# Optimization experiments

Hardware: AMD Instinct MI355X
Metric: run time of the kernel (lower is better)

The kernel has to match this reference:

```python
import jax, jax.numpy as jnp
import numpy as np

D, HS, HE, E, K = 1024, 2048, 1024, 8, 2   # d_model, shared hidden (d_ff//2), expert hidden (d_ff//4), n_experts, top_k
B, T = 4, 1024
N_SHARED = 1


def setup_inputs() -> dict:
    key = jax.random.key(0)
    ks = jax.random.split(key, 9)
    g = lambda k, shape, s: jax.random.normal(k, shape, jnp.float32) * s
    return {
        "x": g(ks[0], (B, T, D), 1.0),
        "t_emb": g(ks[1], (B, D), 1.0),
        "router_W": g(ks[2], (2 * D, E), 0.01),      # torch Linear(2C->E, bias=False), std=0.01 init
        "router_bias": jnp.zeros((E,), jnp.float32),  # load-balance bias buffer
        "w1": g(ks[3], (D, HS), 0.02),                # shared expert SwiGLU
        "w3": g(ks[4], (D, HS), 0.02),
        "w2": g(ks[5], (HS, D), 0.02),
        "W1e": g(ks[6], (E, D, HE), 0.02),            # routed experts, Linear->GELU->Linear
        "W2e": g(ks[7], (E, HE, D), 0.02),
    }


def reference(x, t_emb, router_W, router_bias, w1, w3, w2, W1e, W2e):
    Bb, Tt, C = x.shape
    xf = x.reshape(-1, C)                                              # [N, C]
    tf = jnp.broadcast_to(t_emb[:, None, :], (Bb, Tt, C)).reshape(-1, C)
    N = xf.shape[0]

    shared = (jax.nn.silu(xf @ w1) * (xf @ w3)) @ w2                   # [N, C]

    # router affinity (sigmoid, fp32)
    s = jax.nn.sigmoid((jnp.concatenate([xf, tf], axis=-1) @ router_W).astype(jnp.float32))
    sel_scores = s + router_bias                                       # [N, E]
    _, topk_idx = jax.lax.top_k(sel_scores, K)                         # [N, K]

    # gates normalized over selected raw affinities
    s_sel = jnp.take_along_axis(s, topk_idx, axis=1)                   # [N, K]
    denom = s_sel.sum(axis=1, keepdims=True)
    gates = jnp.where(denom > 1e-9, s_sel / (denom + 1e-9), 1.0 / K).astype(x.dtype)

    # combine weights [N, E]: scatter gates to selected experts
    combine = jnp.zeros((N, E), x.dtype).at[jnp.arange(N)[:, None], topk_idx].add(gates)

    # dense expert evaluation (reference form of grouped GEMM + scatter-combine)
    h = jax.nn.gelu(jnp.einsum('nc,ech->enh', xf, W1e), approximate=False)  # [E, N, He]
    y = jnp.einsum('enh,ehc->enc', h, W2e)                                   # [E, N, C]
    routed = jnp.einsum('ne,enc->nc', combine, y)                            # [N, C]

    return ((shared + routed) / (N_SHARED + K)).reshape(Bb, Tt, C)
```

## Files before the change

kernel.cpp:

```cpp
#include <hip/hip_runtime.h>
#include <hip/hip_bf16.h>
#include <math.h>

#define D_MODEL 1024
#define HS 2048
#define HE 1024
#define NEXP 8
#define NTOK 4096
#define NSLOT 8192

typedef __attribute__((ext_vector_type(4))) float f32x4;
typedef __attribute__((ext_vector_type(8))) short bf16x8;

__device__ __forceinline__ short f2b(float f) {
  __hip_bfloat16 h = __float2bfloat16(f);
  return *reinterpret_cast<short*>(&h);
}
__device__ __forceinline__ float b2f(short s) {
  return __bfloat162float(*reinterpret_cast<__hip_bfloat16*>(&s));
}

__device__ __forceinline__ void gl_lds16(const short* g, short* l) {
  __builtin_amdgcn_global_load_lds(
      (const __attribute__((address_space(1))) void*)g,
      (__attribute__((address_space(3))) void*)l, 16, 0, 0);
}

__device__ __forceinline__ void tr_tile(const float* __restrict__ in,
                                        short* __restrict__ out, int R, int C,
                                        int bx, int by, int bz, int rmap,
                                        float (*tile)[69], int t) {
  const int c0 = bx * 64;
  const int r0 = by * 64;
  const size_t bo = (size_t)bz * R * C;
  const int lr = t >> 4;
  const int lc4 = (t & 15) * 4;
#pragma unroll
  for (int i = 0; i < 4; i++) {
    const float4 v = *(const float4*)&in[bo + (size_t)(r0 + lr + i * 16) * C + c0 + lc4];
    tile[lc4 + 0][lr + i * 16] = v.x;
    tile[lc4 + 1][lr + i * 16] = v.y;
    tile[lc4 + 2][lr + i * 16] = v.z;
    tile[lc4 + 3][lr + i * 16] = v.w;
  }
  __syncthreads();
#pragma unroll
  for (int i = 0; i < 4; i++) {
    const int oc = (t >> 4) + i * 16;
    const int or4 = (t & 15) * 4;
    short4 o;
    o.x = f2b(tile[oc][or4 + 0]);
    o.y = f2b(tile[oc][or4 + 1]);
    o.z = f2b(tile[oc][or4 + 2]);
    o.w = f2b(tile[oc][or4 + 3]);
    const int c = c0 + oc;
    size_t orow;
    if (rmap == 0) orow = bo + (size_t)c * R;
    else orow = (size_t)((c >> 5) * 64 + (rmap == 2 ? 32 : 0) + (c & 31)) * R;
    *(short4*)&out[orow + r0 + or4] = o;
  }
}

__global__ __launch_bounds__(256) void tr_w13(const float* __restrict__ w1,
                                              const float* __restrict__ w3,
                                              short* __restrict__ w13I) {
  __shared__ float tile[64][69];
  const int z = blockIdx.z;
  tr_tile(z ? w3 : w1, w13I, D_MODEL, HS, blockIdx.x, blockIdx.y, 0, z ? 2 : 1,
          tile, threadIdx.x);
}

__global__ __launch_bounds__(256) void tr_w2(const float* __restrict__ w2,
                                             short* __restrict__ w2T) {
  __shared__ float tile[64][69];
  tr_tile(w2, w2T, HS, D_MODEL, blockIdx.x, blockIdx.y, 0, 0, tile, threadIdx.x);
}

__global__ __launch_bounds__(256) void tr_exp(const float* __restrict__ W1e,
                                              const float* __restrict__ W2e,
                                              short* __restrict__ W1eT,
                                              short* __restrict__ W2eT) {
  __shared__ float tile[64][69];
  const int z = blockIdx.z;
  if (z < 8)
    tr_tile(W1e, W1eT, D_MODEL, HE, blockIdx.x, blockIdx.y, z, 0, tile, threadIdx.x);
  else
    tr_tile(W2e, W2eT, HE, D_MODEL, blockIdx.x, blockIdx.y, z - 8, 0, tile, threadIdx.x);
}

__global__ __launch_bounds__(256) void router_kernel(
    const float* __restrict__ x, const float* __restrict__ temb,
    const float* __restrict__ rw, const float* __restrict__ rbias,
    short* __restrict__ xb, int* __restrict__ topk, float* __restrict__ gates) {
  const int t = (blockIdx.x * 256 + threadIdx.x) >> 6;
  const int lane = threadIdx.x & 63;
  const float* xr = x + (size_t)t * D_MODEL;
  const float* tr = temb + (size_t)(t >> 10) * D_MODEL;
  float acc[NEXP] = {};
#pragma unroll
  for (int i = 0; i < 4; i++) {
    const int j = i * 256 + lane * 4;
    const float4 xv = *(const float4*)&xr[j];
    const float4 tv = *(const float4*)&tr[j];
    short4 o;
    o.x = f2b(xv.x); o.y = f2b(xv.y); o.z = f2b(xv.z); o.w = f2b(xv.w);
    *(short4*)&xb[(size_t)t * D_MODEL + j] = o;
    const float* wx = rw + (size_t)j * NEXP;
    const float* wt = rw + (size_t)(D_MODEL + j) * NEXP;
    const float xa[4] = {xv.x, xv.y, xv.z, xv.w};
    const float ta[4] = {tv.x, tv.y, tv.z, tv.w};
#pragma unroll
    for (int u = 0; u < 4; u++)
#pragma unroll
      for (int e = 0; e < NEXP; e++)
        acc[e] += xa[u] * wx[u * NEXP + e] + ta[u] * wt[u * NEXP + e];
  }
#pragma unroll
  for (int off = 32; off; off >>= 1)
#pragma unroll
    for (int e = 0; e < NEXP; e++) acc[e] += __shfl_xor(acc[e], off);
  if (lane == 0) {
    float s[NEXP], sel[NEXP];
#pragma unroll
    for (int e = 0; e < NEXP; e++) {
      s[e] = 1.f / (1.f + expf(-acc[e]));
      sel[e] = s[e] + rbias[e];
    }
    int i0 = 0;
#pragma unroll
    for (int e = 1; e < NEXP; e++) if (sel[e] > sel[i0]) i0 = e;
    int i1 = (i0 == 0) ? 1 : 0;
#pragma unroll
    for (int e = 0; e < NEXP; e++) if (e != i0 && sel[e] > sel[i1]) i1 = e;
    float s0 = s[i0], s1 = s[i1], den = s0 + s1;
    float g0, g1;
    if (den > 1e-9f) { g0 = s0 / (den + 1e-9f); g1 = s1 / (den + 1e-9f); }
    else { g0 = 0.5f; g1 = 0.5f; }
    topk[t * 2] = i0; topk[t * 2 + 1] = i1;
    gates[t * 2] = g0; gates[t * 2 + 1] = g1;
  }
}

__global__ __launch_bounds__(1024) void group_kernel(const int* __restrict__ topk,
                                                     int* __restrict__ perm,
                                                     int* __restrict__ offs,
                                                     int* __restrict__ te,
                                                     int* __restrict__ tm,
                                                     int* __restrict__ ntile) {
  __shared__ int cnt[NEXP], cur[NEXP];
  const int t = threadIdx.x;
  if (t < NEXP) cnt[t] = 0;
  __syncthreads();
  int mye[8];
#pragma unroll
  for (int i = 0; i < 8; i++) {
    mye[i] = topk[i * 1024 + t];
    atomicAdd(&cnt[mye[i]], 1);
  }
  __syncthreads();
  if (t == 0) {
    int a = 0;
    for (int e = 0; e < NEXP; e++) { offs[e] = a; cur[e] = a; a += cnt[e]; }
    offs[NEXP] = a;
    int nt = 0;
    for (int e = 0; e < NEXP; e++)
      for (int m0 = 0; m0 < cnt[e]; m0 += 128) { te[nt] = e; tm[nt] = m0; nt++; }
    ntile[0] = nt;
  }
  __syncthreads();
#pragma unroll
  for (int i = 0; i < 8; i++) {
    int pos = atomicAdd(&cur[mye[i]], 1);
    perm[pos] = i * 1024 + t;
  }
}

template <int MODE, int NT>
__global__ __launch_bounds__(256, 2) void g128(
    const short* __restrict__ A, const short* __restrict__ B, void* __restrict__ Cout,
    const int* __restrict__ perm, const int* __restrict__ offs,
    const float* __restrict__ gates, const int* __restrict__ te,
    const int* __restrict__ tm, const int* __restrict__ ntile,
    const short* __restrict__ yb) {
  extern __shared__ short lds[];
  const int td = threadIdx.x;
  const int K = NT * 64;

  int m_panel = 0, n_panel = 0, e = 0, m0 = 0, rbeg = 0, rend = 0, bxn = 0;
  const short* Bbase;
  if (MODE == 0) {
    const int xcd = blockIdx.x & 7, w = blockIdx.x >> 3;
    n_panel = xcd * 4 + (w >> 5);
    m_panel = w & 31;
    Bbase = B + (size_t)n_panel * 128 * K;
  } else if (MODE == 3) {
    const int xcd = blockIdx.x & 7, slot = blockIdx.x >> 3;
    n_panel = slot & 7;
    m_panel = xcd * 4 + (slot >> 3);
    Bbase = B + (size_t)n_panel * 128 * K;
  } else {
    const int ty = blockIdx.x >> 3;
    if (ty >= ntile[0]) return;
    bxn = blockIdx.x & 7;
    e = te[ty];
    m0 = tm[ty];
    rbeg = offs[e]; rend = offs[e + 1];
    Bbase = B + ((size_t)e * 1024 + bxn * 128) * K;
  }

  const int srow = td >> 3;
  const int colsw8 = ((td & 7) ^ (srow & 7)) * 8;
  const short* ap[4];
  const short* bp[4];
#pragma unroll
  for (int u = 0; u < 4; u++) {
    const int trow = u * 32 + srow;
    int grow;
    if (MODE == 0) grow = m_panel * 128 + trow;
    else if (MODE == 1) grow = perm[min(rbeg + m0 + trow, rend - 1)] >> 1;
    else if (MODE == 2) grow = min(rbeg + m0 + trow, rend - 1);
    else grow = m_panel * 128 + trow;
    ap[u] = A + (size_t)grow * K + colsw8;
    bp[u] = Bbase + (size_t)trow * K + colsw8;
  }

#define STAGE(t_, b_)                                                      \
  do {                                                                     \
    gl_lds16(ap[0] + (t_) * 64, lds + (b_) * 16384 + td * 8);              \
    gl_lds16(ap[1] + (t_) * 64, lds + (b_) * 16384 + 2048 + td * 8);       \
    gl_lds16(ap[2] + (t_) * 64, lds + (b_) * 16384 + 4096 + td * 8);       \
    gl_lds16(ap[3] + (t_) * 64, lds + (b_) * 16384 + 6144 + td * 8);       \
    gl_lds16(bp[0] + (t_) * 64, lds + (b_) * 16384 + 8192 + td * 8);       \
    gl_lds16(bp[1] + (t_) * 64, lds + (b_) * 16384 + 10240 + td * 8);      \
    gl_lds16(bp[2] + (t_) * 64, lds + (b_) * 16384 + 12288 + td * 8);      \
    gl_lds16(bp[3] + (t_) * 64, lds + (b_) * 16384 + 14336 + td * 8);      \
  } while (0)

  const int l = td & 63;
  const int wv = td >> 6;
  const int wm = (wv >> 1) * 64, wn = (wv & 1) * 64;
  const int lr = l & 15;
  const int swzk0 = ((0 + (l >> 4) * 16) ^ ((l & 7) << 4)) >> 1;
  const int swzk1 = ((64 + (l >> 4) * 16) ^ ((l & 7) << 4)) >> 1;

#define LDA(mf_, swz_) (*(const bf16x8*)&Ah[(unsigned)(((mf_)*16 + lr) * 64) + (swz_)])
#define LDB(nf_, swz_) (*(const bf16x8*)&Bh[(unsigned)(((nf_)*16 + lr) * 64) + (swz_)])
#define MMROW(mf_, a_)                                                                 \
  acc[mf_][0] = __builtin_amdgcn_mfma_f32_16x16x32_bf16(a_, b0, acc[mf_][0], 0, 0, 0); \
  acc[mf_][1] = __builtin_amdgcn_mfma_f32_16x16x32_bf16(a_, b1, acc[mf_][1], 0, 0, 0); \
  acc[mf_][2] = __builtin_amdgcn_mfma_f32_16x16x32_bf16(a_, b2, acc[mf_][2], 0, 0, 0); \
  acc[mf_][3] = __builtin_amdgcn_mfma_f32_16x16x32_bf16(a_, b3, acc[mf_][3], 0, 0, 0)

  f32x4 acc[4][4] = {};

  STAGE(0, 0);
  for (int t = 0; t < NT; ++t) {
    const int p = t & 1, q = p ^ 1;
    const short* Ah = lds + p * 16384 + wm * 64;
    const short* Bh = lds + p * 16384 + 8192 + wn * 64;
    if (t < NT - 1) {
      STAGE(t + 1, q);
      asm volatile("s_waitcnt vmcnt(8)" ::: "memory");
    } else {
      asm volatile("s_waitcnt vmcnt(0)" ::: "memory");
    }
    __builtin_amdgcn_s_barrier();
    {
      bf16x8 b0, b1, b2, b3, a0, a1, a2, a3;
      b0 = LDB(0, swzk0); b1 = LDB(1, swzk0); b2 = LDB(2, swzk0); b3 = LDB(3, swzk0);
      a0 = LDA(0, swzk0); a1 = LDA(1, swzk0); a2 = LDA(2, swzk0); a3 = LDA(3, swzk0);
      __builtin_amdgcn_s_setprio(1);
      MMROW(0, a0); MMROW(1, a1); MMROW(2, a2); MMROW(3, a3);
      __builtin_amdgcn_s_setprio(0);
      b0 = LDB(0, swzk1); b1 = LDB(1, swzk1); b2 = LDB(2, swzk1); b3 = LDB(3, swzk1);
      a0 = LDA(0, swzk1); a1 = LDA(1, swzk1); a2 = LDA(2, swzk1); a3 = LDA(3, swzk1);
      __builtin_amdgcn_s_setprio(1);
      MMROW(0, a0); MMROW(1, a1); MMROW(2, a2); MMROW(3, a3);
      __builtin_amdgcn_s_setprio(0);
    }
    __builtin_amdgcn_sched_barrier(0);
    __builtin_amdgcn_s_barrier();
  }

  const int rq = (l >> 4) * 4;
  if (MODE == 0) {
#pragma unroll
    for (int mf = 0; mf < 4; mf++)
#pragma unroll
      for (int j = 0; j < 4; j++) {
        const int row = m_panel * 128 + wm + mf * 16 + rq + j;
        short* Up = (short*)Cout + (size_t)row * HS + n_panel * 64 + (wn >> 1) + lr;
#pragma unroll
        for (int nf = 0; nf < 2; nf++) {
          const float a = acc[mf][nf][j];
          const float b = acc[mf][nf + 2][j];
          Up[nf * 16] = f2b(a / (1.f + expf(-a)) * b);
        }
      }
  } else if (MODE == 1) {
#pragma unroll
    for (int mf = 0; mf < 4; mf++)
#pragma unroll
      for (int j = 0; j < 4; j++) {
        const int gi = rbeg + m0 + wm + mf * 16 + rq + j;
        if (gi < rend) {
          short* Cp = (short*)Cout + (size_t)gi * HE + bxn * 128 + wn + lr;
#pragma unroll
          for (int nf = 0; nf < 4; nf++) {
            const float v = acc[mf][nf][j];
            Cp[nf * 16] = f2b(0.5f * v * (1.0f + erff(v * 0.70710678118654752f)));
          }
        }
      }
  } else if (MODE == 2) {
#pragma unroll
    for (int mf = 0; mf < 4; mf++)
#pragma unroll
      for (int j = 0; j < 4; j++) {
        const int gi = rbeg + m0 + wm + mf * 16 + rq + j;
        if (gi < rend) {
          const int slot = perm[gi];
          const float g = gates[slot];
          short* Cp = (short*)Cout + (size_t)slot * D_MODEL + bxn * 128 + wn + lr;
#pragma unroll
          for (int nf = 0; nf < 4; nf++) Cp[nf * 16] = f2b(g * acc[mf][nf][j]);
        }
      }
  } else {
    const float inv3 = 1.0f / 3.0f;
#pragma unroll
    for (int mf = 0; mf < 4; mf++)
#pragma unroll
      for (int j = 0; j < 4; j++) {
        const int tok = m_panel * 128 + wm + mf * 16 + rq + j;
        const int colb = n_panel * 128 + wn + lr;
        const short* y0p = yb + (size_t)(tok * 2) * D_MODEL + colb;
        const short* y1p = yb + (size_t)(tok * 2 + 1) * D_MODEL + colb;
        float* Op = (float*)Cout + (size_t)tok * D_MODEL + colb;
#pragma unroll
        for (int nf = 0; nf < 4; nf++) {
          Op[nf * 16] = (acc[mf][nf][j] + b2f(y0p[nf * 16]) + b2f(y1p[nf * 16])) * inv3;
        }
      }
  }
#undef STAGE
#undef LDA
#undef LDB
#undef MMROW
}

extern "C" void kernel_launch(void* const* d_in, const int* in_sizes, int n_in,
                              void* d_out, int out_size, void* d_ws, size_t ws_size,
                              hipStream_t stream) {
  const float* x = (const float*)d_in[0];
  const float* temb = (const float*)d_in[1];
  const float* rw = (const float*)d_in[2];
  const float* rbias = (const float*)d_in[3];
  const float* w1 = (const float*)d_in[4];
  const float* w3 = (const float*)d_in[5];
  const float* w2 = (const float*)d_in[6];
  const float* W1e = (const float*)d_in[7];
  const float* W2e = (const float*)d_in[8];
  float* out = (float*)d_out;

  const size_t MB = 1ull << 20;
  char* w = (char*)d_ws;
  short* xb    = (short*)(w + 0 * MB);
  short* w13I  = (short*)(w + 8 * MB);
  short* w2T   = (short*)(w + 16 * MB);
  short* W1eT  = (short*)(w + 20 * MB);
  short* W2eT  = (short*)(w + 36 * MB);
  short* ubuf  = (short*)(w + 52 * MB);
  short* hexpb = (short*)(w + 68 * MB);
  short* yb    = (short*)(w + 84 * MB);
  float* gates = (float*)(w + 100 * MB);
  int* topk    = (int*)(w + 100 * MB + 32 * 1024);
  int* perm    = (int*)(w + 100 * MB + 64 * 1024);
  int* meta    = (int*)(w + 100 * MB + 96 * 1024);
  int* offs    = meta;
  int* te      = meta + 16;
  int* tm      = meta + 128;
  int* ntile   = meta + 256;

  hipFuncSetAttribute((const void*)&g128<0, 16>,
                      hipFuncAttributeMaxDynamicSharedMemorySize, 65536);
  hipFuncSetAttribute((const void*)&g128<1, 16>,
                      hipFuncAttributeMaxDynamicSharedMemorySize, 65536);
  hipFuncSetAttribute((const void*)&g128<2, 16>,
                      hipFuncAttributeMaxDynamicSharedMemorySize, 65536);
  hipFuncSetAttribute((const void*)&g128<3, 32>,
                      hipFuncAttributeMaxDynamicSharedMemorySize, 65536);

  tr_w13<<<dim3(HS / 64, D_MODEL / 64, 2), 256, 0, stream>>>(w1, w3, w13I);
  tr_w2<<<dim3(D_MODEL / 64, HS / 64, 1), 256, 0, stream>>>(w2, w2T);
  tr_exp<<<dim3(16, 16, 16), 256, 0, stream>>>(W1e, W2e, W1eT, W2eT);
  router_kernel<<<NTOK / 4, 256, 0, stream>>>(x, temb, rw, rbias, xb, topk, gates);
  group_kernel<<<1, 1024, 0, stream>>>(topk, perm, offs, te, tm, ntile);

  g128<0, 16><<<1024, 256, 65536, stream>>>(xb, w13I, ubuf, nullptr, nullptr,
                                            nullptr, nullptr, nullptr, nullptr, nullptr);

  g128<1, 16><<<576, 256, 65536, stream>>>(xb, W1eT, hexpb, perm, offs, gates,
                                           te, tm, ntile, nullptr);
  g128<2, 16><<<576, 256, 65536, stream>>>(hexpb, W2eT, yb, perm, offs, gates,
                                           te, tm, ntile, nullptr);

  g128<3, 32><<<256, 256, 65536, stream>>>(ubuf, w2T, out, nullptr, nullptr,
                                           nullptr, nullptr, nullptr, nullptr, yb);
}
```

Measured before the change: 225.7 us.

## Merge GEMM launches into combined shared+routed kernels with smaller-K tiles

Merges the three weight-transpose kernels into one launch. The shared up-projection and routed expert first GEMM now run in one grid, using a BK=32 tile with 32KB LDS and 4 blocks per CU. The shared down-projection and expert second GEMM also share one grid, and a separate elementwise kernel adds the routed outputs. This aims to fill the GPU better and cut launch tails, at the cost of an extra read-modify-write pass over the fp32 output and twice as many K-loop barriers in the first GEMM.

```diff
diff --git a/kernel.cpp b/kernel.cpp
--- a/kernel.cpp
+++ b/kernel.cpp
@@ -61,31 +61,28 @@
   }
 }
 
-__global__ __launch_bounds__(256) void tr_w13(const float* __restrict__ w1,
-                                              const float* __restrict__ w3,
-                                              short* __restrict__ w13I) {
+__global__ __launch_bounds__(256) void tr_all(
+    const float* __restrict__ w1, const float* __restrict__ w3,
+    const float* __restrict__ w2, const float* __restrict__ W1e,
+    const float* __restrict__ W2e, short* __restrict__ w13I,
+    short* __restrict__ w2T, short* __restrict__ W1eT, short* __restrict__ W2eT) {
   __shared__ float tile[64][69];
-  const int z = blockIdx.z;
-  tr_tile(z ? w3 : w1, w13I, D_MODEL, HS, blockIdx.x, blockIdx.y, 0, z ? 2 : 1,
-          tile, threadIdx.x);
-}
-
-__global__ __launch_bounds__(256) void tr_w2(const float* __restrict__ w2,
-                                             short* __restrict__ w2T) {
-  __shared__ float tile[64][69];
-  tr_tile(w2, w2T, HS, D_MODEL, blockIdx.x, blockIdx.y, 0, 0, tile, threadIdx.x);
-}
-
-__global__ __launch_bounds__(256) void tr_exp(const float* __restrict__ W1e,
-                                              const float* __restrict__ W2e,
-                                              short* __restrict__ W1eT,
-                                              short* __restrict__ W2eT) {
-  __shared__ float tile[64][69];
-  const int z = blockIdx.z;
-  if (z < 8)
-    tr_tile(W1e, W1eT, D_MODEL, HE, blockIdx.x, blockIdx.y, z, 0, tile, threadIdx.x);
-  else
-    tr_tile(W2e, W2eT, HE, D_MODEL, blockIdx.x, blockIdx.y, z - 8, 0, tile, threadIdx.x);
+  const int id = blockIdx.x;
+  const int t = threadIdx.x;
+  if (id < 1024) {
+    const int z = id >> 9, rem = id & 511;
+    tr_tile(z ? w3 : w1, w13I, D_MODEL, HS, rem & 31, rem >> 5, 0, z ? 2 : 1, tile, t);
+  } else if (id < 1536) {
+    const int rem = id - 1024;
+    tr_tile(w2, w2T, HS, D_MODEL, rem & 15, rem >> 4, 0, 0, tile, t);
+  } else {
+    const int rem = id - 1536;
+    const int z = rem >> 8, r2 = rem & 255;
+    if (z < 8)
+      tr_tile(W1e, W1eT, D_MODEL, HE, r2 & 15, r2 >> 4, z, 0, tile, t);
+    else
+      tr_tile(W2e, W2eT, HE, D_MODEL, r2 & 15, r2 >> 4, z - 8, 0, tile, t);
+  }
 }
 
 __global__ __launch_bounds__(256) void router_kernel(
@@ -175,37 +172,172 @@
   }
 }
 
-template <int MODE, int NT>
-__global__ __launch_bounds__(256, 2) void g128(
-    const short* __restrict__ A, const short* __restrict__ B, void* __restrict__ Cout,
+__global__ __launch_bounds__(256, 4) void moe_k1(
+    const short* __restrict__ xb, const short* __restrict__ w13I,
+    const short* __restrict__ W1eT, short* __restrict__ ubuf,
+    short* __restrict__ hexpb, const int* __restrict__ perm,
+    const int* __restrict__ offs, const int* __restrict__ te,
+    const int* __restrict__ tm, const int* __restrict__ ntile) {
+  extern __shared__ short lds[];
+  const int td = threadIdx.x;
+  const int id = blockIdx.x;
+  const bool isG1 = id < 1024;
+  int m_panel = 0, n_panel = 0, m0 = 0, rbeg = 0, rend = 0, bxn = 0;
+  const short* A;
+  const short* Bb;
+  if (isG1) {
+    const int xcd = id & 7, w = id >> 3;
+    n_panel = xcd * 4 + (w >> 5);
+    m_panel = w & 31;
+    A = xb;
+    Bb = w13I + (size_t)n_panel * 128 * 1024;
+  } else {
+    const int g = id - 1024;
+    const int ty = g >> 3;
+    if (ty >= ntile[0]) return;
+    bxn = g & 7;
+    const int e = te[ty];
+    m0 = tm[ty];
+    rbeg = offs[e]; rend = offs[e + 1];
+    A = xb;
+    Bb = W1eT + ((size_t)e * 1024 + bxn * 128) * 1024;
+  }
+
+  const int srow = td >> 2;
+  const int colsw = ((td & 3) ^ ((td >> 4) & 3)) * 8;
+  const short* a0p;
+  const short* a1p;
+  {
+    int g0, g1;
+    if (isG1) { g0 = m_panel * 128 + srow; g1 = g0 + 64; }
+    else {
+      g0 = perm[min(rbeg + m0 + srow, rend - 1)] >> 1;
+      g1 = perm[min(rbeg + m0 + 64 + srow, rend - 1)] >> 1;
+    }
+    a0p = A + (size_t)g0 * 1024 + colsw;
+    a1p = A + (size_t)g1 * 1024 + colsw;
+  }
+  const short* b0p = Bb + (size_t)srow * 1024 + colsw;
+  const short* b1p = Bb + (size_t)(64 + srow) * 1024 + colsw;
+
+#define K1STAGE(t_, b_)                                             \
+  do {                                                              \
+    gl_lds16(a0p + (t_) * 32, lds + (b_) * 8192 + td * 8);          \
+    gl_lds16(a1p + (t_) * 32, lds + (b_) * 8192 + 2048 + td * 8);   \
+    gl_lds16(b0p + (t_) * 32, lds + (b_) * 8192 + 4096 + td * 8);   \
+    gl_lds16(b1p + (t_) * 32, lds + (b_) * 8192 + 6144 + td * 8);   \
+  } while (0)
+
+  const int l = td & 63;
+  const int wv = td >> 6;
+  const int wm = (wv >> 1) * 64, wn = (wv & 1) * 64;
+  const int lr = l & 15;
+  const int kg = l >> 4;
+
+#define SWO(r_) ((unsigned)((r_) * 32 + ((kg ^ (((r_) >> 2) & 3)) * 8)))
+#define LDA1(mf_) (*(const bf16x8*)&Ah[SWO(wm + (mf_)*16 + lr)])
+#define LDB1(nf_) (*(const bf16x8*)&Bh[SWO(wn + (nf_)*16 + lr)])
+#define MM1(mf_, a_)                                                                   \
+  acc[mf_][0] = __builtin_amdgcn_mfma_f32_16x16x32_bf16(a_, b0, acc[mf_][0], 0, 0, 0); \
+  acc[mf_][1] = __builtin_amdgcn_mfma_f32_16x16x32_bf16(a_, b1, acc[mf_][1], 0, 0, 0); \
+  acc[mf_][2] = __builtin_amdgcn_mfma_f32_16x16x32_bf16(a_, b2, acc[mf_][2], 0, 0, 0); \
+  acc[mf_][3] = __builtin_amdgcn_mfma_f32_16x16x32_bf16(a_, b3, acc[mf_][3], 0, 0, 0)
+
+  f32x4 acc[4][4] = {};
+
+  K1STAGE(0, 0);
+  for (int t = 0; t < 32; ++t) {
+    const int p = t & 1, q = p ^ 1;
+    const short* Ah = lds + p * 8192;
+    const short* Bh = lds + p * 8192 + 4096;
+    if (t < 31) {
+      K1STAGE(t + 1, q);
+      asm volatile("s_waitcnt vmcnt(4)" ::: "memory");
+    } else {
+      asm volatile("s_waitcnt vmcnt(0)" ::: "memory");
+    }
+    __builtin_amdgcn_s_barrier();
+    {
+      bf16x8 b0 = LDB1(0), b1 = LDB1(1), b2 = LDB1(2), b3 = LDB1(3);
+      bf16x8 a0 = LDA1(0), a1 = LDA1(1), a2 = LDA1(2), a3 = LDA1(3);
+      __builtin_amdgcn_s_setprio(1);
+      MM1(0, a0); MM1(1, a1); MM1(2, a2); MM1(3, a3);
+      __builtin_amdgcn_s_setprio(0);
+    }
+    __builtin_amdgcn_sched_barrier(0);
+    __builtin_amdgcn_s_barrier();
+  }
+
+  const int rq = (l >> 4) * 4;
+  if (isG1) {
+#pragma unroll
+    for (int mf = 0; mf < 4; mf++)
+#pragma unroll
+      for (int j = 0; j < 4; j++) {
+        const int row = m_panel * 128 + wm + mf * 16 + rq + j;
+        short* Up = ubuf + (size_t)row * HS + n_panel * 64 + (wn >> 1) + lr;
+#pragma unroll
+        for (int nf = 0; nf < 2; nf++) {
+          const float a = acc[mf][nf][j];
+          const float b = acc[mf][nf + 2][j];
+          Up[nf * 16] = f2b(a / (1.f + expf(-a)) * b);
+        }
+      }
+  } else {
+#pragma unroll
+    for (int mf = 0; mf < 4; mf++)
+#pragma unroll
+      for (int j = 0; j < 4; j++) {
+        const int gi = rbeg + m0 + wm + mf * 16 + rq + j;
+        if (gi < rend) {
+          short* Cp = hexpb + (size_t)gi * HE + bxn * 128 + wn + lr;
+#pragma unroll
+          for (int nf = 0; nf < 4; nf++) {
+            const float v = acc[mf][nf][j];
+            Cp[nf * 16] = f2b(0.5f * v * (1.0f + erff(v * 0.70710678118654752f)));
+          }
+        }
+      }
+  }
+#undef K1STAGE
+#undef SWO
+#undef LDA1
+#undef LDB1
+#undef MM1
+}
+
+__global__ __launch_bounds__(256, 2) void moe_k2(
+    const short* __restrict__ ubuf, const short* __restrict__ w2T,
+    const short* __restrict__ hexpb, const short* __restrict__ W2eT,
+    float* __restrict__ out, short* __restrict__ yb,
     const int* __restrict__ perm, const int* __restrict__ offs,
     const float* __restrict__ gates, const int* __restrict__ te,
-    const int* __restrict__ tm, const int* __restrict__ ntile,
-    const short* __restrict__ yb) {
+    const int* __restrict__ tm, const int* __restrict__ ntile) {
   extern __shared__ short lds[];
   const int td = threadIdx.x;
-  const int K = NT * 64;
-
-  int m_panel = 0, n_panel = 0, e = 0, m0 = 0, rbeg = 0, rend = 0, bxn = 0;
-  const short* Bbase;
-  if (MODE == 0) {
-    const int xcd = blockIdx.x & 7, w = blockIdx.x >> 3;
-    n_panel = xcd * 4 + (w >> 5);
-    m_panel = w & 31;
-    Bbase = B + (size_t)n_panel * 128 * K;
-  } else if (MODE == 3) {
-    const int xcd = blockIdx.x & 7, slot = blockIdx.x >> 3;
+  const int id = blockIdx.x;
+  const bool isG2 = id < 256;
+  int m_panel = 0, n_panel = 0, m0 = 0, rbeg = 0, rend = 0, bxn = 0, NT, K;
+  const short* A;
+  const short* Bb;
+  if (isG2) {
+    const int xcd = id & 7, slot = id >> 3;
     n_panel = slot & 7;
     m_panel = xcd * 4 + (slot >> 3);
-    Bbase = B + (size_t)n_panel * 128 * K;
+    A = ubuf;
+    K = HS; NT = 32;
+    Bb = w2T + (size_t)n_panel * 128 * HS;
   } else {
-    const int ty = blockIdx.x >> 3;
+    const int g = id - 256;
+    const int ty = g >> 3;
     if (ty >= ntile[0]) return;
-    bxn = blockIdx.x & 7;
-    e = te[ty];
+    bxn = g & 7;
+    const int e = te[ty];
     m0 = tm[ty];
     rbeg = offs[e]; rend = offs[e + 1];
-    Bbase = B + ((size_t)e * 1024 + bxn * 128) * K;
+    A = hexpb;
+    K = HE; NT = 16;
+    Bb = W2eT + ((size_t)e * 1024 + bxn * 128) * 1024;
   }
 
   const int srow = td >> 3;
@@ -216,15 +348,13 @@
   for (int u = 0; u < 4; u++) {
     const int trow = u * 32 + srow;
     int grow;
-    if (MODE == 0) grow = m_panel * 128 + trow;
-    else if (MODE == 1) grow = perm[min(rbeg + m0 + trow, rend - 1)] >> 1;
-    else if (MODE == 2) grow = min(rbeg + m0 + trow, rend - 1);
-    else grow = m_panel * 128 + trow;
+    if (isG2) grow = m_panel * 128 + trow;
+    else grow = min(rbeg + m0 + trow, rend - 1);
     ap[u] = A + (size_t)grow * K + colsw8;
-    bp[u] = Bbase + (size_t)trow * K + colsw8;
-  }
-
-#define STAGE(t_, b_)                                                      \
+    bp[u] = Bb + (size_t)trow * K + colsw8;
+  }
+
+#define K2STAGE(t_, b_)                                                    \
   do {                                                                     \
     gl_lds16(ap[0] + (t_) * 64, lds + (b_) * 16384 + td * 8);              \
     gl_lds16(ap[1] + (t_) * 64, lds + (b_) * 16384 + 2048 + td * 8);       \
@@ -243,9 +373,9 @@
   const int swzk0 = ((0 + (l >> 4) * 16) ^ ((l & 7) << 4)) >> 1;
   const int swzk1 = ((64 + (l >> 4) * 16) ^ ((l & 7) << 4)) >> 1;
 
-#define LDA(mf_, swz_) (*(const bf16x8*)&Ah[(unsigned)(((mf_)*16 + lr) * 64) + (swz_)])
-#define LDB(nf_, swz_) (*(const bf16x8*)&Bh[(unsigned)(((nf_)*16 + lr) * 64) + (swz_)])
-#define MMROW(mf_, a_)                                                                 \
+#define LDA2(mf_, swz_) (*(const bf16x8*)&Ah[(unsigned)(((mf_)*16 + lr) * 64) + (swz_)])
+#define LDB2(nf_, swz_) (*(const bf16x8*)&Bh[(unsigned)(((nf_)*16 + lr) * 64) + (swz_)])
+#define MM2(mf_, a_)                                                                   \
   acc[mf_][0] = __builtin_amdgcn_mfma_f32_16x16x32_bf16(a_, b0, acc[mf_][0], 0, 0, 0); \
   acc[mf_][1] = __builtin_amdgcn_mfma_f32_16x16x32_bf16(a_, b1, acc[mf_][1], 0, 0, 0); \
   acc[mf_][2] = __builtin_amdgcn_mfma_f32_16x16x32_bf16(a_, b2, acc[mf_][2], 0, 0, 0); \
@@ -253,13 +383,13 @@
 
   f32x4 acc[4][4] = {};
 
-  STAGE(0, 0);
+  K2STAGE(0, 0);
   for (int t = 0; t < NT; ++t) {
     const int p = t & 1, q = p ^ 1;
     const short* Ah = lds + p * 16384 + wm * 64;
     const short* Bh = lds + p * 16384 + 8192 + wn * 64;
     if (t < NT - 1) {
-      STAGE(t + 1, q);
+      K2STAGE(t + 1, q);
       asm volatile("s_waitcnt vmcnt(8)" ::: "memory");
     } else {
       asm volatile("s_waitcnt vmcnt(0)" ::: "memory");
@@ -267,15 +397,15 @@
     __builtin_amdgcn_s_barrier();
     {
       bf16x8 b0, b1, b2, b3, a0, a1, a2, a3;
-      b0 = LDB(0, swzk0); b1 = LDB(1, swzk0); b2 = LDB(2, swzk0); b3 = LDB(3, swzk0);
-      a0 = LDA(0, swzk0); a1 = LDA(1, swzk0); a2 = LDA(2, swzk0); a3 = LDA(3, swzk0);
+      b0 = LDB2(0, swzk0); b1 = LDB2(1, swzk0); b2 = LDB2(2, swzk0); b3 = LDB2(3, swzk0);
+      a0 = LDA2(0, swzk0); a1 = LDA2(1, swzk0); a2 = LDA2(2, swzk0); a3 = LDA2(3, swzk0);
       __builtin_amdgcn_s_setprio(1);
-      MMROW(0, a0); MMROW(1, a1); MMROW(2, a2); MMROW(3, a3);
+      MM2(0, a0); MM2(1, a1); MM2(2, a2); MM2(3, a3);
       __builtin_amdgcn_s_setprio(0);
-      b0 = LDB(0, swzk1); b1 = LDB(1, swzk1); b2 = LDB(2, swzk1); b3 = LDB(3, swzk1);
-      a0 = LDA(0, swzk1); a1 = LDA(1, swzk1); a2 = LDA(2, swzk1); a3 = LDA(3, swzk1);
+      b0 = LDB2(0, swzk1); b1 = LDB2(1, swzk1); b2 = LDB2(2, swzk1); b3 = LDB2(3, swzk1);
+      a0 = LDA2(0, swzk1); a1 = LDA2(1, swzk1); a2 = LDA2(2, swzk1); a3 = LDA2(3, swzk1);
       __builtin_amdgcn_s_setprio(1);
-      MMROW(0, a0); MMROW(1, a1); MMROW(2, a2); MMROW(3, a3);
+      MM2(0, a0); MM2(1, a1); MM2(2, a2); MM2(3, a3);
       __builtin_amdgcn_s_setprio(0);
     }
     __builtin_amdgcn_sched_barrier(0);
@@ -283,36 +413,17 @@
   }
 
   const int rq = (l >> 4) * 4;
-  if (MODE == 0) {
+  if (isG2) {
 #pragma unroll
     for (int mf = 0; mf < 4; mf++)
 #pragma unroll
       for (int j = 0; j < 4; j++) {
-        const int row = m_panel * 128 + wm + mf * 16 + rq + j;
-        short* Up = (short*)Cout + (size_t)row * HS + n_panel * 64 + (wn >> 1) + lr;
-#pragma unroll
-        for (int nf = 0; nf < 2; nf++) {
-          const float a = acc[mf][nf][j];
-          const float b = acc[mf][nf + 2][j];
-          Up[nf * 16] = f2b(a / (1.f + expf(-a)) * b);
-        }
+        const int tok = m_panel * 128 + wm + mf * 16 + rq + j;
+        float* Op = out + (size_t)tok * D_MODEL + n_panel * 128 + wn + lr;
+#pragma unroll
+        for (int nf = 0; nf < 4; nf++) Op[nf * 16] = acc[mf][nf][j];
       }
-  } else if (MODE == 1) {
-#pragma unroll
-    for (int mf = 0; mf < 4; mf++)
-#pragma unroll
-      for (int j = 0; j < 4; j++) {
-        const int gi = rbeg + m0 + wm + mf * 16 + rq + j;
-        if (gi < rend) {
-          short* Cp = (short*)Cout + (size_t)gi * HE + bxn * 128 + wn + lr;
-#pragma unroll
-          for (int nf = 0; nf < 4; nf++) {
-            const float v = acc[mf][nf][j];
-            Cp[nf * 16] = f2b(0.5f * v * (1.0f + erff(v * 0.70710678118654752f)));
-          }
-        }
-      }
-  } else if (MODE == 2) {
+  } else {
 #pragma unroll
     for (int mf = 0; mf < 4; mf++)
 #pragma unroll
@@ -321,32 +432,36 @@
         if (gi < rend) {
           const int slot = perm[gi];
           const float g = gates[slot];
-          short* Cp = (short*)Cout + (size_t)slot * D_MODEL + bxn * 128 + wn + lr;
+          short* Cp = yb + (size_t)slot * D_MODEL + bxn * 128 + wn + lr;
 #pragma unroll
           for (int nf = 0; nf < 4; nf++) Cp[nf * 16] = f2b(g * acc[mf][nf][j]);
         }
       }
-  } else {
-    const float inv3 = 1.0f / 3.0f;
-#pragma unroll
-    for (int mf = 0; mf < 4; mf++)
-#pragma unroll
-      for (int j = 0; j < 4; j++) {
-        const int tok = m_panel * 128 + wm + mf * 16 + rq + j;
-        const int colb = n_panel * 128 + wn + lr;
-        const short* y0p = yb + (size_t)(tok * 2) * D_MODEL + colb;
-        const short* y1p = yb + (size_t)(tok * 2 + 1) * D_MODEL + colb;
-        float* Op = (float*)Cout + (size_t)tok * D_MODEL + colb;
-#pragma unroll
-        for (int nf = 0; nf < 4; nf++) {
-          Op[nf * 16] = (acc[mf][nf][j] + b2f(y0p[nf * 16]) + b2f(y1p[nf * 16])) * inv3;
-        }
-      }
-  }
-#undef STAGE
-#undef LDA
-#undef LDB
-#undef MMROW
+  }
+#undef K2STAGE
+#undef LDA2
+#undef LDB2
+#undef MM2
+}
+
+__global__ __launch_bounds__(256) void combine_kernel(float* __restrict__ out,
+                                                      const short* __restrict__ yb) {
+  const float inv3 = 1.0f / 3.0f;
+#pragma unroll
+  for (int rep = 0; rep < 2; rep++) {
+    const int i = (rep * 2048 + blockIdx.x) * 256 + threadIdx.x;
+    const int base = i * 4;
+    const int tok = base >> 10;
+    const int col = base & (D_MODEL - 1);
+    float4 s = *(float4*)&out[base];
+    const short4 y0 = *(const short4*)&yb[(size_t)(tok * 2) * D_MODEL + col];
+    const short4 y1 = *(const short4*)&yb[(size_t)(tok * 2 + 1) * D_MODEL + col];
+    s.x = (s.x + b2f(y0.x) + b2f(y1.x)) * inv3;
+    s.y = (s.y + b2f(y0.y) + b2f(y1.y)) * inv3;
+    s.z = (s.z + b2f(y0.z) + b2f(y1.z)) * inv3;
+    s.w = (s.w + b2f(y0.w) + b2f(y1.w)) * inv3;
+    *(float4*)&out[base] = s;
+  }
 }
 
 extern "C" void kernel_launch(void* const* d_in, const int* in_sizes, int n_in,
@@ -382,29 +497,20 @@
   int* tm      = meta + 128;
   int* ntile   = meta + 256;
 
-  hipFuncSetAttribute((const void*)&g128<0, 16>,
+  hipFuncSetAttribute((const void*)&moe_k1,
+                      hipFuncAttributeMaxDynamicSharedMemorySize, 32768);
+  hipFuncSetAttribute((const void*)&moe_k2,
                       hipFuncAttributeMaxDynamicSharedMemorySize, 65536);
-  hipFuncSetAttribute((const void*)&g128<1, 16>,
-                      hipFuncAttributeMaxDynamicSharedMemorySize, 65536);
-  hipFuncSetAttribute((const void*)&g128<2, 16>,
-                      hipFuncAttributeMaxDynamicSharedMemorySize, 65536);
-  hipFuncSetAttribute((const void*)&g128<3, 32>,
-                      hipFuncAttributeMaxDynamicSharedMemorySize, 65536);
-
-  tr_w13<<<dim3(HS / 64, D_MODEL / 64, 2), 256, 0, stream>>>(w1, w3, w13I);
-  tr_w2<<<dim3(D_MODEL / 64, HS / 64, 1), 256, 0, stream>>>(w2, w2T);
-  tr_exp<<<dim3(16, 16, 16), 256, 0, stream>>>(W1e, W2e, W1eT, W2eT);
+
+  tr_all<<<5632, 256, 0, stream>>>(w1, w3, w2, W1e, W2e, w13I, w2T, W1eT, W2eT);
   router_kernel<<<NTOK / 4, 256, 0, stream>>>(x, temb, rw, rbias, xb, topk, gates);
   group_kernel<<<1, 1024, 0, stream>>>(topk, perm, offs, te, tm, ntile);
 
-  g128<0, 16><<<1024, 256, 65536, stream>>>(xb, w13I, ubuf, nullptr, nullptr,
-                                            nullptr, nullptr, nullptr, nullptr, nullptr);
-
-  g128<1, 16><<<576, 256, 65536, stream>>>(xb, W1eT, hexpb, perm, offs, gates,
-                                           te, tm, ntile, nullptr);
-  g128<2, 16><<<576, 256, 65536, stream>>>(hexpb, W2eT, yb, perm, offs, gates,
-                                           te, tm, ntile, nullptr);
-
-  g128<3, 32><<<256, 256, 65536, stream>>>(ubuf, w2T, out, nullptr, nullptr,
-                                           nullptr, nullptr, nullptr, nullptr, yb);
-}
+  moe_k1<<<1600, 256, 32768, stream>>>(xb, w13I, W1eT, ubuf, hexpb, perm, offs,
+                                       te, tm, ntile);
+
+  moe_k2<<<832, 256, 65536, stream>>>(ubuf, w2T, hexpb, W2eT, out, yb, perm,
+                                      offs, gates, te, tm, ntile);
+
+  combine_kernel<<<2048, 256, 0, stream>>>(out, yb);
+}
```

After: 210.8 us. -6.6%, faster.
